# Performance work log

Hardware: AMD Instinct MI355X
Metric: run time of the kernel (lower is better)

## Reference

```python
import jax, jax.numpy as jnp
import numpy as np

B, S, D = 32, 257, 1024
H, HD = 16, 64
E, R, K = 8, 16, 2
SCALE = HD ** -0.5


def _lora_linear(x, w_fixed, A_all, B_all, bias, idx, gates):
    # x: [B,S,D]; w_fixed: [O,D]; A_all: [E,R,D]; B_all: [E,O,R]; idx: [B,K]; gates: [B,K]
    base = jnp.einsum('bsd,od->bso', x, w_fixed)
    A_sel = A_all[idx]  # [B,K,R,D] per-sample expert gather
    B_sel = B_all[idx]  # [B,K,O,R]
    xa = jnp.einsum('bsd,bkrd->bksr', x, A_sel)          # low-rank down-proj
    expert = jnp.einsum('bksr,bkor,bk->bso', xa, B_sel, gates)
    return base + expert + bias


def setup_inputs() -> dict:
    key = jax.random.key(0)
    ks = jax.random.split(key, 20)
    inp = {
        'hidden_states': jax.random.normal(ks[0], (B, S, D), jnp.float32),
        'top_k_indices': jax.random.randint(ks[1], (B, K), 0, E),
        'top_k_gates': jax.random.uniform(ks[2], (B, K), jnp.float32),
    }
    i = 3
    for name in ('q', 'k', 'v', 'o'):
        inp[f'w{name}_fixed'] = jax.random.normal(ks[i], (D, D), jnp.float32) * 0.02; i += 1
        inp[f'A_{name}'] = jax.random.normal(ks[i], (E, R, D), jnp.float32) * 0.02; i += 1
        inp[f'B_{name}'] = jax.random.normal(ks[i], (E, D, R), jnp.float32) * 0.02; i += 1
        inp[f'b_{name}'] = jnp.zeros((D,), jnp.float32)
    return inp


def reference(hidden_states, top_k_indices, top_k_gates,
              wq_fixed, A_q, B_q, b_q,
              wk_fixed, A_k, B_k, b_k,
              wv_fixed, A_v, B_v, b_v,
              wo_fixed, A_o, B_o, b_o):
    idx, gates = top_k_indices, top_k_gates
    q = _lora_linear(hidden_states, wq_fixed, A_q, B_q, b_q, idx, gates) * SCALE
    k = _lora_linear(hidden_states, wk_fixed, A_k, B_k, b_k, idx, gates)
    v = _lora_linear(hidden_states, wv_fixed, A_v, B_v, b_v, idx, gates)
    # [B,S,D] -> [B,H,S,HD]
    q = q.reshape(B, S, H, HD).transpose(0, 2, 1, 3)
    k = k.reshape(B, S, H, HD).transpose(0, 2, 1, 3)
    v = v.reshape(B, S, H, HD).transpose(0, 2, 1, 3)
    attn = jax.nn.softmax(jnp.einsum('bhsd,bhtd->bhst', q, k), axis=-1)
    out = jnp.einsum('bhst,bhtd->bhsd', attn, v)
    out = out.transpose(0, 2, 1, 3).reshape(B, S, D)
    return _lora_linear(out, wo_fixed, A_o, B_o, b_o, idx, gates)
```

## Files before the change

### kernel.cpp

```cpp
#include <hip/hip_runtime.h>


#define BB 32
#define SS 257
#define DD 1024
#define HH 16
#define HDIM 64
#define EE 8
#define RR 16
#define MTOT (BB * SS)
#define MPAD 8448
#define VTS 264

typedef __attribute__((ext_vector_type(8))) _Float16 f16x8;
typedef __attribute__((ext_vector_type(4))) float f32x4;

static __device__ __forceinline__ float4 ld4(const float* p) {
    return *(const float4*)p;
}
static __device__ __forceinline__ unsigned short f16b(float x) {
    union { _Float16 f; unsigned short u; } cv;
    cv.f = (_Float16)x;
    return cv.u;
}

static __device__ __forceinline__ void gl_lds16(const unsigned short* g,
                                                unsigned short* l) {
    __builtin_amdgcn_global_load_lds(
        (const __attribute__((address_space(1))) unsigned int*)g,
        (__attribute__((address_space(3))) unsigned int*)l, 16, 0, 0);
}

static __device__ __forceinline__ int xcd_swz(int orig, int nwg) {
    const int xcd = orig & 7;
    const int lin = orig >> 3;
    const int q = nwg >> 3;
    const int r = nwg & 7;
    return (xcd < r ? xcd * (q + 1) : r * (q + 1) + (xcd - r) * q) + lin;
}

__global__ __launch_bounds__(256) void prep(
    const float* __restrict__ hidden, const float* __restrict__ wq,
    const float* __restrict__ wk, const float* __restrict__ wv,
    const float* __restrict__ wo, const float* __restrict__ Aq,
    const float* __restrict__ Ak, const float* __restrict__ Av,
    const float* __restrict__ Ao, const float* __restrict__ Bq,
    const float* __restrict__ Bk, const float* __restrict__ Bv,
    const float* __restrict__ Bo, const int* __restrict__ tki,
    const float* __restrict__ tkg, unsigned short* __restrict__ Xf,
    unsigned short* __restrict__ Wcat, unsigned short* __restrict__ Who,
    unsigned short* __restrict__ A3, unsigned short* __restrict__ Ao16,
    unsigned short* __restrict__ Bccat, unsigned short* __restrict__ Bco)
{
    const int tid = threadIdx.x;
    int bx = blockIdx.x;
    if (bx < 8448) {
        long i = ((long)bx * 256 + tid) * 4;
        float4 v = (i < (long)MTOT * DD) ? ld4(&hidden[i])
                                         : make_float4(0.f, 0.f, 0.f, 0.f);
        ushort4 hv;
        hv.x = f16b(v.x); hv.y = f16b(v.y); hv.z = f16b(v.z); hv.w = f16b(v.w);
        *(ushort4*)&Xf[i] = hv;
        return;
    }
    bx -= 8448;
    if (bx < 4096) {
        const int sel = bx >> 10;
        long i = ((long)(bx & 1023) * 256 + tid) * 4;
        const float* src = (sel == 0) ? wq : (sel == 1) ? wk
                                          : (sel == 2) ? wv : wo;
        unsigned short* dst =
            (sel < 3) ? Wcat + (size_t)sel * DD * DD : Who;
        float4 v = ld4(&src[i]);
        ushort4 hv;
        hv.x = f16b(v.x); hv.y = f16b(v.y); hv.z = f16b(v.z); hv.w = f16b(v.w);
        *(ushort4*)&dst[i] = hv;
        return;
    }
    bx -= 4096;
    if (bx < 512) {
        const int sel = bx >> 7;
        long i = ((long)(bx & 127) * 256 + tid) * 4;
        const float* src = (sel == 0) ? Aq : (sel == 1) ? Ak
                                          : (sel == 2) ? Av : Ao;
        unsigned short* dst =
            (sel < 3) ? A3 + (size_t)sel * EE * RR * DD : Ao16;
        float4 v = ld4(&src[i]);
        ushort4 hv;
        hv.x = f16b(v.x); hv.y = f16b(v.y); hv.z = f16b(v.z); hv.w = f16b(v.w);
        *(ushort4*)&dst[i] = hv;
        return;
    }
    bx -= 512;
    {
        const int set = bx >> 8;
        const int i = (bx & 255) * 256 + tid;
        const int b = i >> 11;
        const int rem = i & 2047;
        const int n = rem >> 1;
        const int ke = rem & 1;
        const float* Ball = (set == 0) ? Bq : (set == 1) ? Bk
                                           : (set == 2) ? Bv : Bo;
        const int e = tki[b * 2 + ke];
        const float g = tkg[b * 2 + ke];
        const float* sp = &Ball[((size_t)e * DD + n) * RR];
        unsigned short o16[16];
#pragma unroll
        for (int r4 = 0; r4 < 4; ++r4) {
            float4 v = ld4(sp + r4 * 4);
            o16[r4 * 4 + 0] = f16b(g * v.x);
            o16[r4 * 4 + 1] = f16b(g * v.y);
            o16[r4 * 4 + 2] = f16b(g * v.z);
            o16[r4 * 4 + 3] = f16b(g * v.w);
        }
        unsigned short* dst =
            (set < 3) ? &Bccat[((size_t)b * 3072 + set * 1024 + n) * 32 + ke * 16]
                      : &Bco[((size_t)b * 1024 + n) * 32 + ke * 16];
        *(uint4*)&dst[0] = *(uint4*)&o16[0];
        *(uint4*)&dst[8] = *(uint4*)&o16[8];
    }
}

#define COMPUTE1()                                                             \
    do {                                                                       \
        f16x8 af[4], bf[4];                                                    \
        const int sb = (quad ^ ((l16 >> 1) & 3)) * 8;                          \
        _Pragma("unroll") for (int t = 0; t < 4; ++t) {                        \
            af[t] = *(const f16x8*)&Ah[(wm + t * 16 + l16) * 32 + sb];         \
            bf[t] = *(const f16x8*)&Bh[(wn + t * 16 + l16) * 32 + sb];         \
        }                                                                      \
        _Pragma("unroll") for (int i = 0; i < 4; ++i)                          \
        _Pragma("unroll") for (int j = 0; j < 4; ++j)                          \
            acc[i][j] = __builtin_amdgcn_mfma_f32_16x16x32_f16(                \
                af[i], bf[j], acc[i][j], 0, 0, 0);                             \
    } while (0)

__global__ __launch_bounds__(256) void gemm_xa(
    const unsigned short* __restrict__ Xf, const unsigned short* __restrict__ A0,
    const unsigned short* __restrict__ A1, const unsigned short* __restrict__ A2,
    unsigned short* __restrict__ XA, int ncols)
{
    __shared__ unsigned short Ah[128 * 32];
    __shared__ unsigned short Bh[128 * 32];
    const int tid = threadIdx.x;
    const int m0 = blockIdx.y * 128;
    const int p = blockIdx.x;
    const unsigned short* Ap = (p == 0) ? A0 : (p == 1) ? A1 : A2;
    const int lane = tid & 63;
    const int w = tid >> 6;
    const int wm = (w >> 1) * 64;
    const int wn = (w & 1) * 64;
    const int l16 = lane & 15;
    const int quad = lane >> 4;

    f32x4 acc[4][4];
#pragma unroll
    for (int i = 0; i < 4; ++i)
#pragma unroll
        for (int j = 0; j < 4; ++j) acc[i][j] = (f32x4){0.f, 0.f, 0.f, 0.f};

    const int srow = tid >> 2;
    const int scol = (((tid & 3) ^ ((tid >> 3) & 3))) * 8;
    const int lbase = (tid & 192) * 8;
    const size_t xr0 = (size_t)(m0 + srow) * DD + scol;
    const size_t xr1 = (size_t)(m0 + srow + 64) * DD + scol;
    const size_t ar0 = (size_t)srow * DD + scol;
    const size_t ar1 = (size_t)(srow + 64) * DD + scol;

#pragma unroll 1
    for (int kt = 0; kt < 32; ++kt) {
        const int k0 = kt * 32;
        gl_lds16(Xf + xr0 + k0, &Ah[lbase]);
        gl_lds16(Xf + xr1 + k0, &Ah[2048 + lbase]);
        gl_lds16(Ap + ar0 + k0, &Bh[lbase]);
        gl_lds16(Ap + ar1 + k0, &Bh[2048 + lbase]);
        __syncthreads();
        COMPUTE1();
        __syncthreads();
    }

#pragma unroll
    for (int j = 0; j < 4; ++j) {
        const int col = p * 128 + wn + j * 16 + l16;
#pragma unroll
        for (int i = 0; i < 4; ++i) {
            const int mb = m0 + wm + i * 16 + quad * 4;
#pragma unroll
            for (int rg = 0; rg < 4; ++rg) {
                const int m = mb + rg;
                if (m < MTOT)
                    XA[(size_t)m * ncols + col] = f16b(acc[i][j][rg]);
            }
        }
    }
}

#define QKV_STAGE(BUFI, KT)                                                    \
    do {                                                                       \
        unsigned short* dA_ = S + (BUFI) * 16384 + w * 512;                    \
        const int k0_ = (KT) * 32;                                             \
        gl_lds16(Xf + gA + k0_, dA_);                                          \
        gl_lds16(Wcat + gB + k0_, dA_ + 8192);                                 \
    } while (0)

#define QKV_PHASES(BUFI)                                                       \
    do {                                                                       \
        const unsigned short* Ab_ = S + (BUFI) * 16384;                        \
        const unsigned short* Bb_ = Ab_ + 8192;                                \
        f16x8 af_[4], bf_[4];                                                  \
        _Pragma("unroll") for (int j = 0; j < 4; ++j)                          \
            bf_[j] = *(const f16x8*)&Bb_[boff + j * 512];                      \
        _Pragma("unroll") for (int i = 0; i < 4; ++i)                          \
            af_[i] = *(const f16x8*)&Ab_[aoff + i * 512];                      \
        __builtin_amdgcn_s_setprio(1);                                         \
        _Pragma("unroll") for (int i = 0; i < 4; ++i)                          \
        _Pragma("unroll") for (int j = 0; j < 4; ++j)                          \
            acc[i][j] = __builtin_amdgcn_mfma_f32_16x16x32_f16(                \
                af_[i], bf_[j], acc[i][j], 0, 0, 0);                           \
        __builtin_amdgcn_s_setprio(0);                                         \
    } while (0)

#define QKV_SYNC() asm volatile("s_waitcnt vmcnt(0)\n\ts_barrier" ::: "memory")

__global__ __launch_bounds__(1024)
__attribute__((amdgpu_waves_per_eu(4, 8))) void gemm_qkv(
    const unsigned short* __restrict__ Xf, const unsigned short* __restrict__ Wcat,
    const float* __restrict__ bq, const float* __restrict__ bk,
    const float* __restrict__ bv, const unsigned short* __restrict__ XAd,
    const unsigned short* __restrict__ Bccat, const int* __restrict__ idx,
    unsigned short* __restrict__ qh, unsigned short* __restrict__ kh,
    unsigned short* __restrict__ vTg)
{
    __shared__ unsigned short S[32768];
    const int tid = threadIdx.x;
    const int wgid = xcd_swz(blockIdx.x, 396);
    const int bxn = wgid % 12;
    const int m0 = (wgid / 12) * 256;
    const int p = bxn >> 2;
    const int n0g = bxn * 256;
    const int nloc0 = (bxn & 3) * 256;
    const int lane = tid & 63;
    const int w = tid >> 6;
    const int wm = (w >> 2) * 64;
    const int wn = (w & 3) * 64;
    const int l16 = lane & 15;
    const int quad = lane >> 4;
    const int sb = (quad ^ ((l16 >> 1) & 3)) * 8;
    const int aoff = (wm + l16) * 32 + sb;
    const int boff = (wn + l16) * 32 + sb;

    f32x4 acc[4][4];
#pragma unroll
    for (int i = 0; i < 4; ++i)
#pragma unroll
        for (int j = 0; j < 4; ++j) acc[i][j] = (f32x4){0.f, 0.f, 0.f, 0.f};

    const int srow = tid >> 2;
    const int schk = ((tid & 3) ^ ((srow >> 1) & 3)) * 8;
    const size_t gA = (size_t)(m0 + srow) * DD + schk;
    const size_t gB = (size_t)(n0g + srow) * DD + schk;

    QKV_STAGE(0, 0);
#pragma unroll 1
    for (int kt = 0; kt < 32; ++kt) {
        QKV_SYNC();
        if (kt < 31) QKV_STAGE((kt + 1) & 1, kt + 1);
        QKV_PHASES(kt & 1);
    }

    {
        int m_hi = m0 + 255;
        if (m_hi >= MTOT) m_hi = MTOT - 1;
        const int b_first = m0 / SS;
        const int b_last = m_hi / SS;
        const int r = tid >> 2;
        const int cc = tid & 3;
        const int key = (r >> 1) & 3;
        const int g = cc ^ key;
        const uint4 z = make_uint4(0, 0, 0, 0);
#pragma unroll 1
        for (int bp = b_first; bp <= b_last; ++bp) {
            const int gm = m0 + r;
            const bool va = (gm < MTOT) && (gm / SS == bp);
            uint4 av = z;
            if (va) {
                const int e = idx[bp * 2 + (g >> 1)];
                av = *(const uint4*)&XAd[(size_t)gm * 384 + p * 128 +
                                         e * 16 + (g & 1) * 8];
            }
            const size_t bo = ((size_t)bp * 3072 + p * 1024 + nloc0 + r) * 32;
            uint4 bv2 = *(const uint4*)&Bccat[bo + g * 8];
            __syncthreads();
            *(uint4*)&S[r * 32 + cc * 8] = av;
            *(uint4*)&S[8192 + r * 32 + cc * 8] = bv2;
            __syncthreads();
            QKV_PHASES(0);
            __syncthreads();
        }
    }

    unsigned short* Epi = S;
    const float* bias = (p == 0) ? bq : (p == 1) ? bk : bv;
    if (p < 2) {
        const float alpha = (p == 0) ? 0.125f : 1.0f;
        unsigned short* C = (p == 0) ? qh : kh;
#pragma unroll 1
        for (int qtr = 0; qtr < 4; ++qtr) {
            if ((w >> 2) == qtr) {
#pragma unroll
                for (int j = 0; j < 4; ++j) {
                    const int col = wn + j * 16 + l16;
                    const float bvl = bias[nloc0 + col];
#pragma unroll
                    for (int i = 0; i < 4; ++i) {
                        const int ml = i * 16 + quad * 4;
#pragma unroll
                        for (int rg = 0; rg < 4; ++rg)
                            Epi[(ml + rg) * 264 + col] =
                                f16b(alpha * (acc[i][j][rg] + bvl));
                    }
                }
            }
            __syncthreads();
            {
                const int r = tid >> 4;
                const int c = (tid & 15) * 16;
                const int m = m0 + qtr * 64 + r;
                if (m < MTOT) {
#pragma unroll
                    for (int k = 0; k < 2; ++k)
                        *(uint4*)&C[(size_t)m * DD + nloc0 + c + k * 8] =
                            *(const uint4*)&Epi[r * 264 + c + k * 8];
                }
            }
            __syncthreads();
        }
    } else {
#pragma unroll 1
        for (int hh = 0; hh < 4; ++hh) {
            if ((w >> 2) == hh) {
#pragma unroll
                for (int j = 0; j < 4; ++j) {
                    const int col = wn + j * 16 + l16;
                    const float bvl = bias[nloc0 + col];
#pragma unroll
                    for (int i = 0; i < 4; ++i) {
                        const int ml = i * 16 + quad * 4;
                        ushort4 pk;
                        pk.x = f16b(acc[i][j][0] + bvl);
                        pk.y = f16b(acc[i][j][1] + bvl);
                        pk.z = f16b(acc[i][j][2] + bvl);
                        pk.w = f16b(acc[i][j][3] + bvl);
                        *(ushort4*)&Epi[col * 68 + ml] = pk;
                    }
                }
            }
            __syncthreads();
            {
                const int tl = tid & 63;
                const int mg = m0 + hh * 64 + tl;
                if (mg < MTOT) {
                    const int bq2 = mg / SS;
                    const int t = mg - bq2 * SS;
#pragma unroll 4
                    for (int k = 0; k < 16; ++k) {
                        const int nll = (tid >> 6) + k * 16;
                        const int d = nloc0 + nll;
                        vTg[((size_t)(bq2 * HH + (d >> 6)) * HDIM + (d & 63)) *
                                VTS + t] = Epi[nll * 68 + tl];
                    }
                }
            }
            __syncthreads();
        }
    }
}

#define O_STAGE(BUFI, KT)                                                      \
    do {                                                                       \
        unsigned short* b_ = S + (BUFI) * 12288;                               \
        const int k0_ = (KT) * 32;                                             \
        gl_lds16(Xf + gA1 + k0_, b_ + w * 1024);                               \
        gl_lds16(Xf + gA2 + k0_, b_ + w * 1024 + 512);                         \
        gl_lds16(Wh2 + gB + k0_, b_ + 8192 + w * 512);                         \
    } while (0)

#define O_PHASES(BUFI)                                                         \
    do {                                                                       \
        const unsigned short* Ab_ = S + (BUFI) * 12288;                        \
        const unsigned short* Bb_ = Ab_ + 8192;                                \
        f16x8 af_[4], bf_[4];                                                  \
        _Pragma("unroll") for (int j = 0; j < 4; ++j)                          \
            bf_[j] = *(const f16x8*)&Bb_[boff + j * 512];                      \
        _Pragma("unroll") for (int i = 0; i < 4; ++i)                          \
            af_[i] = *(const f16x8*)&Ab_[aoff + i * 512];                      \
        __builtin_amdgcn_s_setprio(1);                                         \
        _Pragma("unroll") for (int i = 0; i < 4; ++i)                          \
        _Pragma("unroll") for (int j = 0; j < 4; ++j)                          \
            acc[i][j] = __builtin_amdgcn_mfma_f32_16x16x32_f16(                \
                af_[i], bf_[j], acc[i][j], 0, 0, 0);                           \
        __builtin_amdgcn_s_setprio(0);                                         \
    } while (0)

__global__ __launch_bounds__(512)
__attribute__((amdgpu_waves_per_eu(2, 8))) void gemm_o(
    const unsigned short* __restrict__ Xf, const unsigned short* __restrict__ Wh2,
    const float* __restrict__ bias, const unsigned short* __restrict__ XAo,
    const unsigned short* __restrict__ Bco, const int* __restrict__ idx,
    float* __restrict__ Cf)
{
    __shared__ unsigned short S[24576];
    const int tid = threadIdx.x;
    const int wgid = xcd_swz(blockIdx.x, 264);
    const int m0 = (wgid >> 3) * 256;
    const int n0 = (wgid & 7) * 128;
    const int lane = tid & 63;
    const int w = tid >> 6;
    const int wm = (w >> 1) * 64;
    const int wn = (w & 1) * 64;
    const int l16 = lane & 15;
    const int quad = lane >> 4;
    const int sb = (quad ^ ((l16 >> 1) & 3)) * 8;
    const int aoff = (wm + l16) * 32 + sb;
    const int boff = (wn + l16) * 32 + sb;

    f32x4 acc[4][4];
#pragma unroll
    for (int i = 0; i < 4; ++i)
#pragma unroll
        for (int j = 0; j < 4; ++j) acc[i][j] = (f32x4){0.f, 0.f, 0.f, 0.f};

    const int rowA1 = w * 32 + (lane >> 2);
    const int chk = lane & 3;
    const int keyA = (rowA1 >> 1) & 3;
    const size_t gA1 = (size_t)(m0 + rowA1) * DD + (chk ^ keyA) * 8;
    const size_t gA2 = gA1 + (size_t)16 * DD;
    const int rowB = w * 16 + (lane >> 2);
    const int keyB = (rowB >> 1) & 3;
    const size_t gB = (size_t)(n0 + rowB) * DD + (chk ^ keyB) * 8;

    O_STAGE(0, 0);
#pragma unroll 1
    for (int kt = 0; kt < 32; ++kt) {
        QKV_SYNC();
        if (kt < 31) O_STAGE((kt + 1) & 1, kt + 1);
        O_PHASES(kt & 1);
    }

    {
        int m_hi = m0 + 255;
        if (m_hi >= MTOT) m_hi = MTOT - 1;
        const int b_first = m0 / SS;
        const int b_last = m_hi / SS;
        const int rA = tid >> 1;
        const int b0 = (tid & 1) * 2;
        const int keyTA = (rA >> 1) & 3;
        const int g0 = b0 ^ keyTA, g1 = (b0 + 1) ^ keyTA;
        const int rB = tid >> 2;
        const int ccB = tid & 3;
        const int gBt = ccB ^ ((rB >> 1) & 3);
        const uint4 z = make_uint4(0, 0, 0, 0);
#pragma unroll 1
        for (int bp = b_first; bp <= b_last; ++bp) {
            const int gm = m0 + rA;
            const bool va = (gm < MTOT) && (gm / SS == bp);
            uint4 av0 = z, av1 = z;
            if (va) {
                const int e0 = idx[bp * 2 + (g0 >> 1)];
                const int e1 = idx[bp * 2 + (g1 >> 1)];
                av0 = *(const uint4*)&XAo[(size_t)gm * 128 + e0 * 16 +
                                          (g0 & 1) * 8];
                av1 = *(const uint4*)&XAo[(size_t)gm * 128 + e1 * 16 +
                                          (g1 & 1) * 8];
            }
            const size_t bo = ((size_t)bp * 1024 + n0 + rB) * 32;
            uint4 bv2 = *(const uint4*)&Bco[bo + gBt * 8];
            __syncthreads();
            *(uint4*)&S[rA * 32 + b0 * 8] = av0;
            *(uint4*)&S[rA * 32 + (b0 + 1) * 8] = av1;
            *(uint4*)&S[8192 + rB * 32 + ccB * 8] = bv2;
            __syncthreads();
            O_PHASES(0);
            __syncthreads();
        }
    }

#pragma unroll
    for (int j = 0; j < 4; ++j) {
        const int n = n0 + wn + j * 16 + l16;
        const float bvl = bias[n];
#pragma unroll
        for (int i = 0; i < 4; ++i) {
            const int mb = m0 + wm + i * 16 + quad * 4;
#pragma unroll
            for (int rg = 0; rg < 4; ++rg) {
                const int m = mb + rg;
                if (m < MTOT) Cf[(size_t)m * DD + n] = acc[i][j][rg] + bvl;
            }
        }
    }
}

__global__ __launch_bounds__(512, 1) void attn_v4(
    const unsigned short* __restrict__ qh, const unsigned short* __restrict__ kh,
    const unsigned short* __restrict__ vT, unsigned short* __restrict__ Xf)
{
    __shared__ unsigned short Ks[288 * 64];
    __shared__ unsigned short Vt[64 * VTS];
    __shared__ unsigned short Qs[64 * 64];
    __shared__ unsigned short Ps[64 * 296];
    __shared__ float sredm[2][64];
    __shared__ float sreds[2][64];

    const int tid = threadIdx.x;
    const int h = blockIdx.x, b = blockIdx.y;
    const int cb = h * HDIM;
    const int lane = tid & 63;
    const int w = tid >> 6;
    const int r0 = (w & 3) * 16;
    const int ch = w >> 2;
    const int l16 = lane & 15;
    const int quad = lane >> 4;

    const size_t kbase = (size_t)(b * SS) * DD + cb;
    {
        const int rr = w * 8 + (lane >> 3);
        const int cg = ((lane & 7) ^ (rr & 7)) * 8;
#pragma unroll
        for (int c = 0; c < 4; ++c)
            gl_lds16(kh + kbase + (size_t)(c * 64 + rr) * DD + cg,
                     &Ks[(c * 64 + w * 8) * 64]);
    }
    if (tid < 256) {
        uint4 z = make_uint4(0, 0, 0, 0);
        if (tid < 8) z = *(const uint4*)&kh[kbase + (size_t)256 * DD + tid * 8];
        *(uint4*)&Ks[256 * 64 + tid * 8] = z;
    }
    {
        const size_t vbase = (size_t)(b * HH + h) * HDIM * VTS;
        for (int i = tid; i < 64 * 33; i += 512) {
            const int r = i / 33;
            const int c = i - r * 33;
            uint4 v = *(const uint4*)&vT[vbase + (size_t)r * VTS + c * 8];
            if (c == 32) { v.x &= 0xFFFFu; v.y = 0; v.z = 0; v.w = 0; }
            *(uint4*)&Vt[r * VTS + c * 8] = v;
        }
    }

#pragma unroll 1
    for (int qt = 0; qt < 5; ++qt) {
        const int s0 = qt * 64;
        __syncthreads();
        {
            int sg = s0 + (tid >> 3);
            if (sg > SS - 1) sg = SS - 1;
            const int cg = ((tid & 7) ^ ((tid >> 3) & 7)) * 8;
            gl_lds16(qh + (size_t)(b * SS + sg) * DD + cb + cg,
                     &Qs[(w * 8) * 64]);
        }
        __syncthreads();

        f32x4 lac[9];
#pragma unroll
        for (int ct = 0; ct < 9; ++ct) lac[ct] = (f32x4){0.f, 0.f, 0.f, 0.f};
#pragma unroll
        for (int kc = 0; kc < 2; ++kc) {
            const int sb = ((kc * 4 + quad) ^ (l16 & 7)) * 8;
            f16x8 af = *(const f16x8*)&Qs[(r0 + l16) * 64 + sb];
#pragma unroll
            for (int ct = 0; ct < 9; ++ct) {
                const int c0 = ch * 144 + ct * 16;
                f16x8 bf = *(const f16x8*)&Ks[(c0 + l16) * 64 + sb];
                lac[ct] = __builtin_amdgcn_mfma_f32_16x16x32_f16(
                    af, bf, lac[ct], 0, 0, 0);
            }
        }
#pragma unroll
        for (int ct = 0; ct < 9; ++ct) {
            const int t = ch * 144 + ct * 16 + l16;
            if (t > SS - 1) {
                lac[ct][0] = -1e30f; lac[ct][1] = -1e30f;
                lac[ct][2] = -1e30f; lac[ct][3] = -1e30f;
            }
        }
        float mx[4] = {-1e30f, -1e30f, -1e30f, -1e30f};
#pragma unroll
        for (int ct = 0; ct < 9; ++ct)
#pragma unroll
            for (int i = 0; i < 4; ++i) mx[i] = fmaxf(mx[i], lac[ct][i]);
#pragma unroll
        for (int o = 1; o < 16; o <<= 1)
#pragma unroll
            for (int i = 0; i < 4; ++i)
                mx[i] = fmaxf(mx[i], __shfl_xor(mx[i], o, 16));
        if (l16 == 0)
#pragma unroll
            for (int i = 0; i < 4; ++i) sredm[ch][r0 + quad * 4 + i] = mx[i];
        __syncthreads();
#pragma unroll
        for (int i = 0; i < 4; ++i)
            mx[i] = fmaxf(mx[i], sredm[1 - ch][r0 + quad * 4 + i]);
        float sm[4] = {0.f, 0.f, 0.f, 0.f};
#pragma unroll
        for (int ct = 0; ct < 9; ++ct)
#pragma unroll
            for (int i = 0; i < 4; ++i) {
                float pv = __expf(lac[ct][i] - mx[i]);
                lac[ct][i] = pv;
                sm[i] += pv;
            }
#pragma unroll
        for (int o = 1; o < 16; o <<= 1)
#pragma unroll
            for (int i = 0; i < 4; ++i) sm[i] += __shfl_xor(sm[i], o, 16);
        if (l16 == 0)
#pragma unroll
            for (int i = 0; i < 4; ++i) sreds[ch][r0 + quad * 4 + i] = sm[i];
        __syncthreads();
        float inv[4];
#pragma unroll
        for (int i = 0; i < 4; ++i)
            inv[i] = 1.f / (sm[i] + sreds[1 - ch][r0 + quad * 4 + i]);
#pragma unroll
        for (int ct = 0; ct < 9; ++ct) {
            const int col = ch * 144 + ct * 16 + l16;
#pragma unroll
            for (int i = 0; i < 4; ++i)
                Ps[(r0 + quad * 4 + i) * 296 + col] =
                    f16b(lac[ct][i] * inv[i]);
        }
        __syncthreads();

        f32x4 oacc[2];
        oacc[0] = (f32x4){0.f, 0.f, 0.f, 0.f};
        oacc[1] = (f32x4){0.f, 0.f, 0.f, 0.f};
#pragma unroll
        for (int tt = 0; tt < 9; ++tt) {
            const int t0 = tt * 32;
            f16x8 pf = *(const f16x8*)&Ps[(r0 + l16) * 296 + t0 + quad * 8];
#pragma unroll
            for (int dt = 0; dt < 2; ++dt) {
                f16x8 bvv = *(const f16x8*)&Vt[(ch * 32 + dt * 16 + l16) * VTS +
                                               t0 + quad * 8];
                oacc[dt] = __builtin_amdgcn_mfma_f32_16x16x32_f16(
                    pf, bvv, oacc[dt], 0, 0, 0);
            }
        }
#pragma unroll
        for (int dt = 0; dt < 2; ++dt)
#pragma unroll
            for (int i = 0; i < 4; ++i) {
                const int srow = s0 + r0 + quad * 4 + i;
                if (srow < SS)
                    Xf[(size_t)(b * SS + srow) * DD + cb + ch * 32 + dt * 16 +
                       l16] = f16b(oacc[dt][i]);
            }
    }
}

extern "C" void kernel_launch(void* const* d_in, const int* in_sizes, int n_in,
                              void* d_out, int out_size, void* d_ws,
                              size_t ws_size, hipStream_t stream)
{
    const float* hidden = (const float*)d_in[0];
    const int* tki = (const int*)d_in[1];
    const float* tkg = (const float*)d_in[2];
    const float* wq = (const float*)d_in[3];
    const float* Aq = (const float*)d_in[4];
    const float* Bq = (const float*)d_in[5];
    const float* bq = (const float*)d_in[6];
    const float* wk = (const float*)d_in[7];
    const float* Ak = (const float*)d_in[8];
    const float* Bk = (const float*)d_in[9];
    const float* bkb = (const float*)d_in[10];
    const float* wv = (const float*)d_in[11];
    const float* Av = (const float*)d_in[12];
    const float* Bv = (const float*)d_in[13];
    const float* bvb = (const float*)d_in[14];
    const float* wo = (const float*)d_in[15];
    const float* Ao = (const float*)d_in[16];
    const float* Bo = (const float*)d_in[17];
    const float* bob = (const float*)d_in[18];
    float* out = (float*)d_out;

    char* ws = (char*)d_ws;
    const size_t NW = (size_t)DD * DD;
    const size_t NA = (size_t)EE * RR * DD;
    unsigned short* Xf = (unsigned short*)ws;    ws += (size_t)MPAD * DD * 2;
    unsigned short* qh = (unsigned short*)ws;    ws += (size_t)MTOT * DD * 2;
    unsigned short* vTg = (unsigned short*)ws;   ws += (size_t)BB * HH * HDIM * VTS * 2;
    unsigned short* Wcat = (unsigned short*)ws;  ws += 3 * NW * 2;
    unsigned short* Who = (unsigned short*)ws;   ws += NW * 2;
    unsigned short* A3 = (unsigned short*)ws;    ws += 3 * NA * 2;
    unsigned short* Ao16 = (unsigned short*)ws;  ws += NA * 2;
    unsigned short* Bccat = (unsigned short*)ws; ws += (size_t)BB * 3072 * 32 * 2;
    unsigned short* Bco = (unsigned short*)ws;   ws += (size_t)BB * 1024 * 32 * 2;
    unsigned short* XAo = (unsigned short*)ws;   ws += (size_t)MTOT * 128 * 2;
    unsigned short* kh = (unsigned short*)d_out;
    unsigned short* XAd = (unsigned short*)((char*)d_out + (size_t)MTOT * DD * 2);

    prep<<<14080, 256, 0, stream>>>(hidden, wq, wk, wv, wo, Aq, Ak, Av, Ao,
                                    Bq, Bk, Bv, Bo, tki, tkg, Xf, Wcat, Who,
                                    A3, Ao16, Bccat, Bco);
    gemm_xa<<<dim3(3, 65), 256, 0, stream>>>(Xf, A3, A3 + NA, A3 + 2 * NA,
                                             XAd, 384);
    gemm_qkv<<<396, 1024, 0, stream>>>(Xf, Wcat, bq, bkb, bvb, XAd,
                                       Bccat, tki, qh, kh, vTg);
    attn_v4<<<dim3(HH, BB), 512, 0, stream>>>(qh, kh, vTg, Xf);
    gemm_xa<<<dim3(1, 65), 256, 0, stream>>>(Xf, Ao16, Ao16, Ao16, XAo, 128);
    gemm_o<<<264, 512, 0, stream>>>(Xf, Who, bob, XAo, Bco, tki, out);
}
```

Baseline: 334.0 us.

## Restructure QKV GEMM to 8 waves with 128x64 warp tiles and 4-stage pipeline

The QKV projection GEMM goes from 16 waves of 64x64 tiles to 8 waves of 128x64 tiles, which doubles per-wave register accumulators and raises A/B fragment reuse. The LDS ring grows from 2 to 4 stages, with 3 tiles prefetched. Each iteration splits its MFMA work into two halves and interleaves the async global-to-LDS stage issues between them, using explicit lgkmcnt waits and sched barriers. The LoRA tail and the epilogues are remapped to the new wave layout. In exchange it uses more LDS and registers, which lowers occupancy, and it adds an extra barrier per iteration.

```diff
diff --git a/kernel.cpp b/kernel.cpp
--- a/kernel.cpp
+++ b/kernel.cpp
@@ -195,15 +195,22 @@
     }
 }
 
-#define QKV_STAGE(BUFI, KT)                                                    \
+#define STG_A(BUFI, KT)                                                        \
     do {                                                                       \
-        unsigned short* dA_ = S + (BUFI) * 16384 + w * 512;                    \
+        unsigned short* d_ = S + (BUFI) * 16384 + w * 1024;                    \
         const int k0_ = (KT) * 32;                                             \
-        gl_lds16(Xf + gA + k0_, dA_);                                          \
-        gl_lds16(Wcat + gB + k0_, dA_ + 8192);                                 \
+        gl_lds16(Xf + gA1 + k0_, d_);                                          \
+        gl_lds16(Xf + gA2 + k0_, d_ + 512);                                    \
     } while (0)
-
-#define QKV_PHASES(BUFI)                                                       \
+#define STG_B(BUFI, KT)                                                        \
+    do {                                                                       \
+        unsigned short* d_ = S + (BUFI) * 16384 + 8192 + w * 1024;             \
+        const int k0_ = (KT) * 32;                                             \
+        gl_lds16(Wcat + gB1 + k0_, d_);                                        \
+        gl_lds16(Wcat + gB2 + k0_, d_ + 512);                                  \
+    } while (0)
+
+#define Q8_PHASES(BUFI, DOSTAGE, KT)                                           \
     do {                                                                       \
         const unsigned short* Ab_ = S + (BUFI) * 16384;                        \
         const unsigned short* Bb_ = Ab_ + 8192;                                \
@@ -211,19 +218,32 @@
         _Pragma("unroll") for (int j = 0; j < 4; ++j)                          \
             bf_[j] = *(const f16x8*)&Bb_[boff + j * 512];                      \
         _Pragma("unroll") for (int i = 0; i < 4; ++i)                          \
-            af_[i] = *(const f16x8*)&Ab_[aoff + i * 512];                      \
+            af_[i] = *(const f16x8*)&Ab_[aoffLo + i * 512];                    \
+        if (DOSTAGE) { STG_A((KT) & 3, KT); }                                  \
+        asm volatile("s_waitcnt lgkmcnt(0)" ::: "memory");                     \
+        __builtin_amdgcn_sched_barrier(0);                                     \
         __builtin_amdgcn_s_setprio(1);                                         \
         _Pragma("unroll") for (int i = 0; i < 4; ++i)                          \
         _Pragma("unroll") for (int j = 0; j < 4; ++j)                          \
             acc[i][j] = __builtin_amdgcn_mfma_f32_16x16x32_f16(                \
                 af_[i], bf_[j], acc[i][j], 0, 0, 0);                           \
         __builtin_amdgcn_s_setprio(0);                                         \
+        __builtin_amdgcn_s_barrier();                                          \
+        _Pragma("unroll") for (int i = 0; i < 4; ++i)                          \
+            af_[i] = *(const f16x8*)&Ab_[aoffLo + 2048 + i * 512];             \
+        if (DOSTAGE) { STG_B((KT) & 3, KT); }                                  \
+        asm volatile("s_waitcnt lgkmcnt(0)" ::: "memory");                     \
+        __builtin_amdgcn_sched_barrier(0);                                     \
+        __builtin_amdgcn_s_setprio(1);                                         \
+        _Pragma("unroll") for (int i = 0; i < 4; ++i)                          \
+        _Pragma("unroll") for (int j = 0; j < 4; ++j)                          \
+            acc[i + 4][j] = __builtin_amdgcn_mfma_f32_16x16x32_f16(            \
+                af_[i], bf_[j], acc[i + 4][j], 0, 0, 0);                       \
+        __builtin_amdgcn_s_setprio(0);                                         \
     } while (0)
 
-#define QKV_SYNC() asm volatile("s_waitcnt vmcnt(0)\n\ts_barrier" ::: "memory")
-
-__global__ __launch_bounds__(1024)
-__attribute__((amdgpu_waves_per_eu(4, 8))) void gemm_qkv(
+__global__ __launch_bounds__(512)
+__attribute__((amdgpu_waves_per_eu(2, 2))) void gemm_qkv(
     const unsigned short* __restrict__ Xf, const unsigned short* __restrict__ Wcat,
     const float* __restrict__ bq, const float* __restrict__ bk,
     const float* __restrict__ bv, const unsigned short* __restrict__ XAd,
@@ -231,7 +251,7 @@
     unsigned short* __restrict__ qh, unsigned short* __restrict__ kh,
     unsigned short* __restrict__ vTg)
 {
-    __shared__ unsigned short S[32768];
+    __shared__ unsigned short S[65536];
     const int tid = threadIdx.x;
     const int wgid = xcd_swz(blockIdx.x, 396);
     const int bxn = wgid % 12;
@@ -241,60 +261,74 @@
     const int nloc0 = (bxn & 3) * 256;
     const int lane = tid & 63;
     const int w = tid >> 6;
-    const int wm = (w >> 2) * 64;
+    const int wm = (w >> 2) * 128;
     const int wn = (w & 3) * 64;
     const int l16 = lane & 15;
     const int quad = lane >> 4;
     const int sb = (quad ^ ((l16 >> 1) & 3)) * 8;
-    const int aoff = (wm + l16) * 32 + sb;
+    const int aoffLo = (wm + l16) * 32 + sb;
     const int boff = (wn + l16) * 32 + sb;
 
-    f32x4 acc[4][4];
-#pragma unroll
-    for (int i = 0; i < 4; ++i)
+    f32x4 acc[8][4];
+#pragma unroll
+    for (int i = 0; i < 8; ++i)
 #pragma unroll
         for (int j = 0; j < 4; ++j) acc[i][j] = (f32x4){0.f, 0.f, 0.f, 0.f};
 
-    const int srow = tid >> 2;
-    const int schk = ((tid & 3) ^ ((srow >> 1) & 3)) * 8;
-    const size_t gA = (size_t)(m0 + srow) * DD + schk;
-    const size_t gB = (size_t)(n0g + srow) * DD + schk;
-
-    QKV_STAGE(0, 0);
+    const int rA = w * 32 + (lane >> 2);
+    const int cA = ((lane & 3) ^ ((rA >> 1) & 3)) * 8;
+    const size_t gA1 = (size_t)(m0 + rA) * DD + cA;
+    const size_t gA2 = gA1 + (size_t)16 * DD;
+    const size_t gB1 = (size_t)(n0g + rA) * DD + cA;
+    const size_t gB2 = gB1 + (size_t)16 * DD;
+
+    STG_A(0, 0); STG_B(0, 0);
+    STG_A(1, 1); STG_B(1, 1);
+    STG_A(2, 2); STG_B(2, 2);
+
 #pragma unroll 1
-    for (int kt = 0; kt < 32; ++kt) {
-        QKV_SYNC();
-        if (kt < 31) QKV_STAGE((kt + 1) & 1, kt + 1);
-        QKV_PHASES(kt & 1);
-    }
+    for (int kt = 0; kt < 30; ++kt) {
+        asm volatile("s_waitcnt vmcnt(8)\n\ts_barrier" ::: "memory");
+        Q8_PHASES(kt & 3, kt < 29, kt + 3);
+    }
+    asm volatile("s_waitcnt vmcnt(4)\n\ts_barrier" ::: "memory");
+    Q8_PHASES(2, 0, 0);
+    asm volatile("s_waitcnt vmcnt(0)\n\ts_barrier" ::: "memory");
+    Q8_PHASES(3, 0, 0);
 
     {
         int m_hi = m0 + 255;
         if (m_hi >= MTOT) m_hi = MTOT - 1;
         const int b_first = m0 / SS;
         const int b_last = m_hi / SS;
-        const int r = tid >> 2;
-        const int cc = tid & 3;
+        const int r = tid >> 1;
         const int key = (r >> 1) & 3;
-        const int g = cc ^ key;
+        const int b0 = (tid & 1) * 2;
         const uint4 z = make_uint4(0, 0, 0, 0);
 #pragma unroll 1
         for (int bp = b_first; bp <= b_last; ++bp) {
             const int gm = m0 + r;
             const bool va = (gm < MTOT) && (gm / SS == bp);
-            uint4 av = z;
+            const int g0 = b0 ^ key, g1 = (b0 + 1) ^ key;
+            uint4 av0 = z, av1 = z;
             if (va) {
-                const int e = idx[bp * 2 + (g >> 1)];
-                av = *(const uint4*)&XAd[(size_t)gm * 384 + p * 128 +
-                                         e * 16 + (g & 1) * 8];
+                const int e0 = idx[bp * 2 + (g0 >> 1)];
+                const int e1 = idx[bp * 2 + (g1 >> 1)];
+                av0 = *(const uint4*)&XAd[(size_t)gm * 384 + p * 128 +
+                                          e0 * 16 + (g0 & 1) * 8];
+                av1 = *(const uint4*)&XAd[(size_t)gm * 384 + p * 128 +
+                                          e1 * 16 + (g1 & 1) * 8];
             }
             const size_t bo = ((size_t)bp * 3072 + p * 1024 + nloc0 + r) * 32;
-            uint4 bv2 = *(const uint4*)&Bccat[bo + g * 8];
-            __syncthreads();
-            *(uint4*)&S[r * 32 + cc * 8] = av;
-            *(uint4*)&S[8192 + r * 32 + cc * 8] = bv2;
-            __syncthreads();
-            QKV_PHASES(0);
+            uint4 bv0 = *(const uint4*)&Bccat[bo + g0 * 8];
+            uint4 bv1 = *(const uint4*)&Bccat[bo + g1 * 8];
+            __syncthreads();
+            *(uint4*)&S[r * 32 + b0 * 8] = av0;
+            *(uint4*)&S[r * 32 + (b0 + 1) * 8] = av1;
+            *(uint4*)&S[8192 + r * 32 + b0 * 8] = bv0;
+            *(uint4*)&S[8192 + r * 32 + (b0 + 1) * 8] = bv1;
+            __syncthreads();
+            Q8_PHASES(0, 0, 0);
             __syncthreads();
         }
     }
@@ -305,14 +339,14 @@
         const float alpha = (p == 0) ? 0.125f : 1.0f;
         unsigned short* C = (p == 0) ? qh : kh;
 #pragma unroll 1
-        for (int qtr = 0; qtr < 4; ++qtr) {
-            if ((w >> 2) == qtr) {
+        for (int half = 0; half < 2; ++half) {
+            if ((w >> 2) == half) {
 #pragma unroll
                 for (int j = 0; j < 4; ++j) {
                     const int col = wn + j * 16 + l16;
                     const float bvl = bias[nloc0 + col];
 #pragma unroll
-                    for (int i = 0; i < 4; ++i) {
+                    for (int i = 0; i < 8; ++i) {
                         const int ml = i * 16 + quad * 4;
 #pragma unroll
                         for (int rg = 0; rg < 4; ++rg)
@@ -323,12 +357,12 @@
             }
             __syncthreads();
             {
-                const int r = tid >> 4;
-                const int c = (tid & 15) * 16;
-                const int m = m0 + qtr * 64 + r;
+                const int r = tid >> 2;
+                const int c = (tid & 3) * 64;
+                const int m = m0 + half * 128 + r;
                 if (m < MTOT) {
 #pragma unroll
-                    for (int k = 0; k < 2; ++k)
+                    for (int k = 0; k < 8; ++k)
                         *(uint4*)&C[(size_t)m * DD + nloc0 + c + k * 8] =
                             *(const uint4*)&Epi[r * 264 + c + k * 8];
                 }
@@ -336,16 +370,17 @@
             __syncthreads();
         }
     } else {
-#pragma unroll 1
+#pragma unroll
         for (int hh = 0; hh < 4; ++hh) {
-            if ((w >> 2) == hh) {
+            if ((w >> 2) == (hh >> 1)) {
 #pragma unroll
                 for (int j = 0; j < 4; ++j) {
                     const int col = wn + j * 16 + l16;
                     const float bvl = bias[nloc0 + col];
 #pragma unroll
-                    for (int i = 0; i < 4; ++i) {
-                        const int ml = i * 16 + quad * 4;
+                    for (int i2 = 0; i2 < 4; ++i2) {
+                        const int i = (hh & 1) * 4 + i2;
+                        const int ml = i2 * 16 + quad * 4;
                         ushort4 pk;
                         pk.x = f16b(acc[i][j][0] + bvl);
                         pk.y = f16b(acc[i][j][1] + bvl);
@@ -363,8 +398,8 @@
                     const int bq2 = mg / SS;
                     const int t = mg - bq2 * SS;
 #pragma unroll 4
-                    for (int k = 0; k < 16; ++k) {
-                        const int nll = (tid >> 6) + k * 16;
+                    for (int k = 0; k < 32; ++k) {
+                        const int nll = (tid >> 6) + k * 8;
                         const int d = nloc0 + nll;
                         vTg[((size_t)(bq2 * HH + (d >> 6)) * HDIM + (d & 63)) *
                                 VTS + t] = Epi[nll * 68 + tl];
@@ -375,6 +410,8 @@
         }
     }
 }
+
+#define QKV_SYNC() asm volatile("s_waitcnt vmcnt(0)\n\ts_barrier" ::: "memory")
 
 #define O_STAGE(BUFI, KT)                                                      \
     do {                                                                       \
@@ -704,8 +741,8 @@
                                     A3, Ao16, Bccat, Bco);
     gemm_xa<<<dim3(3, 65), 256, 0, stream>>>(Xf, A3, A3 + NA, A3 + 2 * NA,
                                              XAd, 384);
-    gemm_qkv<<<396, 1024, 0, stream>>>(Xf, Wcat, bq, bkb, bvb, XAd,
-                                       Bccat, tki, qh, kh, vTg);
+    gemm_qkv<<<396, 512, 0, stream>>>(Xf, Wcat, bq, bkb, bvb, XAd,
+                                      Bccat, tki, qh, kh, vTg);
     attn_v4<<<dim3(HH, BB), 512, 0, stream>>>(qh, kh, vTg, Xf);
     gemm_xa<<<dim3(1, 65), 256, 0, stream>>>(Xf, Ao16, Ao16, Ao16, XAo, 128);
     gemm_o<<<264, 512, 0, stream>>>(Xf, Who, bob, XAo, Bco, tki, out);
```

Result: slower. 343.6 us (+2.9%).

## Double-buffer LDS staging in gemm_xa to overlap loads with MFMA

Applied to the files above, without the earlier changes.

Replaces the single-buffer load/sync/compute/sync loop in the XA down-projection GEMM with a two-stage LDS ping-pong. The next k-tile is issued via global-to-LDS loads before computing the current one, with a single waitcnt+barrier per iteration. This aims to hide global load latency behind MFMA work, at the cost of doubling LDS usage (32KB) and relying on the single barrier to protect buffer reuse.

```diff
diff --git a/kernel.cpp b/kernel.cpp
--- a/kernel.cpp
+++ b/kernel.cpp
@@ -121,13 +121,25 @@
     }
 }
 
-#define COMPUTE1()                                                             \
+#define XA_STAGE(BUFI, KT)                                                     \
     do {                                                                       \
+        unsigned short* base_ = Sx + (BUFI) * 8192;                            \
+        const int k0_ = (KT) * 32;                                             \
+        gl_lds16(Xf + xr0 + k0_, base_ + lbase);                               \
+        gl_lds16(Xf + xr1 + k0_, base_ + 2048 + lbase);                        \
+        gl_lds16(Ap + ar0 + k0_, base_ + 4096 + lbase);                        \
+        gl_lds16(Ap + ar1 + k0_, base_ + 6144 + lbase);                        \
+    } while (0)
+
+#define XA_COMPUTE(BUFI)                                                       \
+    do {                                                                       \
+        const unsigned short* Ab_ = Sx + (BUFI) * 8192;                        \
+        const unsigned short* Bb_ = Ab_ + 4096;                                \
         f16x8 af[4], bf[4];                                                    \
         const int sb = (quad ^ ((l16 >> 1) & 3)) * 8;                          \
         _Pragma("unroll") for (int t = 0; t < 4; ++t) {                        \
-            af[t] = *(const f16x8*)&Ah[(wm + t * 16 + l16) * 32 + sb];         \
-            bf[t] = *(const f16x8*)&Bh[(wn + t * 16 + l16) * 32 + sb];         \
+            af[t] = *(const f16x8*)&Ab_[(wm + t * 16 + l16) * 32 + sb];        \
+            bf[t] = *(const f16x8*)&Bb_[(wn + t * 16 + l16) * 32 + sb];        \
         }                                                                      \
         _Pragma("unroll") for (int i = 0; i < 4; ++i)                          \
         _Pragma("unroll") for (int j = 0; j < 4; ++j)                          \
@@ -135,13 +147,14 @@
                 af[i], bf[j], acc[i][j], 0, 0, 0);                             \
     } while (0)
 
+#define XA_SYNC() asm volatile("s_waitcnt vmcnt(0)\n\ts_barrier" ::: "memory")
+
 __global__ __launch_bounds__(256) void gemm_xa(
     const unsigned short* __restrict__ Xf, const unsigned short* __restrict__ A0,
     const unsigned short* __restrict__ A1, const unsigned short* __restrict__ A2,
     unsigned short* __restrict__ XA, int ncols)
 {
-    __shared__ unsigned short Ah[128 * 32];
-    __shared__ unsigned short Bh[128 * 32];
+    __shared__ unsigned short Sx[16384];
     const int tid = threadIdx.x;
     const int m0 = blockIdx.y * 128;
     const int p = blockIdx.x;
@@ -167,16 +180,12 @@
     const size_t ar0 = (size_t)srow * DD + scol;
     const size_t ar1 = (size_t)(srow + 64) * DD + scol;
 
+    XA_STAGE(0, 0);
 #pragma unroll 1
     for (int kt = 0; kt < 32; ++kt) {
-        const int k0 = kt * 32;
-        gl_lds16(Xf + xr0 + k0, &Ah[lbase]);
-        gl_lds16(Xf + xr1 + k0, &Ah[2048 + lbase]);
-        gl_lds16(Ap + ar0 + k0, &Bh[lbase]);
-        gl_lds16(Ap + ar1 + k0, &Bh[2048 + lbase]);
-        __syncthreads();
-        COMPUTE1();
-        __syncthreads();
+        XA_SYNC();
+        if (kt < 31) XA_STAGE((kt + 1) & 1, kt + 1);
+        XA_COMPUTE(kt & 1);
     }
 
 #pragma unroll
```

Result: faster. 324.8 us (-2.8%).
